# Performance work log

Hardware: AMD Instinct MI355X
Metric: run time of the kernel (lower is better)

The kernel has to match this reference:

```python
import jax, jax.numpy as jnp
import numpy as np
from jax import lax

B, C_IN, H, W = 4, 64, 128, 128
NUM_HIDDEN = 64
KSIZE = 3
DIST = 1
MOVES = 2 * DIST + 1          # 3
MOVESQ = MOVES * MOVES        # 9
TIME_STEPS = 8
LOSS_WEIGHT = 0.01


def _shift(a, dy, dx):
    """out(y, x) = a(y+dy, x+dx), zero outside; dy,dx in {-1,0,1}. a: [..., H, W]."""
    p = jnp.pad(a, [(0, 0)] * (a.ndim - 2) + [(1, 1), (1, 1)])
    h, w = a.shape[-2], a.shape[-1]
    return p[..., 1 + dy:1 + dy + h, 1 + dx:1 + dx + w]


def _gather(o4):
    # gather_kernel[i,0,i//3,i%3]=1 => channel i is o4 shifted by (i//3-1, i%3-1)
    return jnp.stack([_shift(o4, i // MOVES - 1, i % MOVES - 1) for i in range(MOVESQ)], axis=1)


def _merge(hxo):
    # hxo: [B, nh, 9, H, W]; merge_kernel[0, 9-i-1, i//3, i%3]=1 grouped per hidden channel
    # => merged(y,x) = sum_j hxo[:,:,j](y + 1 - j//3, x + 1 - j%3)
    return sum(_shift(hxo[:, :, j], 1 - j // MOVES, 1 - j % MOVES) for j in range(MOVESQ))


def _forward(x, mask, w_ih, b_ih, w_hh, b_hh, w_ho, b_ho):
    b, _, h, w = x.shape
    pad = KSIZE // 2
    i_all = lax.conv_general_dilated(
        x, w_ih, (1, 1), [(pad, pad), (pad, pad)],
        dimension_numbers=("NCHW", "OIHW", "NCHW")) + b_ih[None, :, None, None]
    i_r, i_i, i_n = jnp.split(i_all, 3, axis=1)

    h0 = jnp.zeros((b, NUM_HIDDEN, h, w), x.dtype)
    loss0 = jnp.zeros((b, MOVESQ, h, w), x.dtype)  # scalar init broadcasts to this shape

    def step(carry, _):
        hid, loss = carry
        hh = jnp.einsum("bchw,oc->bohw", hid, w_hh) + b_hh[None, :, None, None]
        h_r, h_i, h_n = jnp.split(hh, 3, axis=1)
        resetgate = jax.nn.sigmoid(i_r + h_r)
        inputgate = jax.nn.sigmoid(i_i + h_i)
        newgate = jnp.tanh(i_n + resetgate * h_n)
        hy = newgate + inputgate * (hid - newgate)
        o = jax.nn.softmax(jnp.einsum("bchw,oc->bohw", hy, w_ho) + b_ho[None, :, None, None], axis=1)
        o4 = o[:, 4]
        diff = (_gather(o4) - o) ** 2 * o
        bce = -jnp.mean(mask * jnp.log(1.0 - o4) + (1.0 - mask) * jnp.log(o4))
        loss = loss + bce + diff * LOSS_WEIGHT
        hxo = jnp.einsum("bchw,bdhw->bcdhw", hy, o)  # [B, nh, 9, H, W]
        h_next = _merge(hxo)
        return (h_next, loss), (h_next, o)

    (_, loss), (hiddens, outs) = lax.scan(step, (h0, loss0), None, length=TIME_STEPS)
    return hiddens, outs, loss


def setup_inputs() -> dict:
    key = jax.random.key(0)
    ks = jax.random.split(key, 8)
    s = 0.05
    return {
        "x": jax.random.normal(ks[0], (B, C_IN, H, W), jnp.float32),
        "mask": jax.random.uniform(ks[1], (B, H, W), jnp.float32),
        "w_ih": jax.random.normal(ks[2], (3 * NUM_HIDDEN, C_IN, KSIZE, KSIZE), jnp.float32) * s,
        "b_ih": jax.random.normal(ks[3], (3 * NUM_HIDDEN,), jnp.float32) * s,
        "w_hh": jax.random.normal(ks[4], (3 * NUM_HIDDEN, NUM_HIDDEN), jnp.float32) * s,
        "b_hh": jax.random.normal(ks[5], (3 * NUM_HIDDEN,), jnp.float32) * s,
        "w_ho": jax.random.normal(ks[6], (MOVESQ, NUM_HIDDEN), jnp.float32) * s,
        "b_ho": jax.random.normal(ks[7], (MOVESQ,), jnp.float32) * s,
    }


def reference(x, mask, w_ih, b_ih, w_hh, b_hh, w_ho, b_ho):
    return _forward(x, mask, w_ih, b_ih, w_hh, b_hh, w_ho, b_ho)
```

## Files before the change

### kernel.cpp

```cpp
#include <hip/hip_runtime.h>

#define NP 16384
#define HID_SZ 4194304
#define O_SZ   589824
#define OUTS_OFF 33554432
#define LOSS_OFF 38273024

#define WS_IALL0 0
#define WS_IALL1 4194304
#define WS_HYA   6291456
#define WS_HYB   8388624
#define WS_WHH   10485792
#define WS_WHOB  10491936
#define WS_BTF   10492448
#define WS_BCEP  10547744
#define WS_BCET  10555936

typedef __attribute__((ext_vector_type(8))) short bf16x8;
typedef __attribute__((ext_vector_type(8))) unsigned short ushort8;
typedef __attribute__((ext_vector_type(4))) unsigned short usht4;
typedef __attribute__((ext_vector_type(4))) float f32x4;

__device__ __forceinline__ float frcp(float x) { return __builtin_amdgcn_rcpf(x); }
__device__ __forceinline__ unsigned short f2bf(float f) {
    unsigned int u = __float_as_uint(f);
    return (unsigned short)((u + 0x7fffu + ((u >> 16) & 1u)) >> 16);
}
__device__ __forceinline__ float bf2f(unsigned short h) {
    return __uint_as_float(((unsigned int)h) << 16);
}
__device__ __forceinline__ int swz_bid(int bid) { return ((bid & 7) << 7) | (bid >> 3); }

__global__ __launch_bounds__(256) void prep_all(const float* __restrict__ x,
                                                const float* __restrict__ w_hh,
                                                const float* __restrict__ w_ho,
                                                const float* __restrict__ w_ih,
                                                unsigned short* __restrict__ xTh,
                                                unsigned short* __restrict__ whhBf,
                                                unsigned short* __restrict__ whoBf,
                                                unsigned short* __restrict__ BTf) {
    const int tid = threadIdx.x;
    if (blockIdx.x < 256) {
        const int p = blockIdx.x * 256 + tid;
        const int b = p >> 14, yx = p & 16383;
        const size_t base = ((size_t)p) << 6;
        for (int ic0 = 0; ic0 < 64; ic0 += 8) {
            ushort8 vh;
#pragma unroll
            for (int j = 0; j < 8; ++j)
                vh[j] = f2bf(x[(((size_t)(b * 64 + ic0 + j)) << 14) + yx]);
            *(ushort8*)(xTh + base + ic0) = vh;
        }
    } else {
        int i = (blockIdx.x - 256) * 256 + tid;
        if (i < 12288) {
            int f = i >> 9, r = i & 511;
            int lane = r >> 3, e = r & 7, lrow = lane & 15, lkq = lane >> 4;
            int ih = f / 12, n = f % 12;
            whhBf[i] = f2bf(w_hh[(n * 16 + lrow) * 64 + ih * 32 + lkq * 8 + e]);
        } else if (i < 13312) {
            int j = i - 12288;
            int f = j >> 9, r = j & 511;
            int lane = r >> 3, e = r & 7, lrow = lane & 15, lkq = lane >> 4;
            whoBf[j] = (lrow < 9) ? f2bf(w_ho[lrow * 64 + f * 32 + lkq * 8 + e]) : (unsigned short)0;
        } else if (i < 13312 + 110592) {
            int k2 = i - 13312;
            int f = k2 >> 9, r = k2 & 511;
            int lane = r >> 3, e = r & 7, lrow = lane & 15, lkq = lane >> 4;
            int tapih = f / 12, n = f % 12;
            int tap = tapih >> 1, ih = tapih & 1;
            int oc = n * 16 + lrow, ic = ih * 32 + lkq * 8 + e;
            BTf[k2] = f2bf(w_ih[(oc * 64 + ic) * 9 + tap]);
        }
    }
}

__global__ __launch_bounds__(256, 4) void conv_mfma(const unsigned short* __restrict__ xTh,
                                                    const unsigned short* __restrict__ BTf,
                                                    const float* __restrict__ b_ih,
                                                    unsigned short* __restrict__ iall0,
                                                    unsigned short* __restrict__ iall1) {
    __shared__ __align__(16) unsigned char smem[25344];
    const int tid = threadIdx.x;
    const int bid = swz_bid(blockIdx.x);
    const int b = bid >> 8, y = (bid >> 1) & 127, hh2 = bid & 1;

    for (int ch = tid; ch < 1584; ch += 256) {
        const int row = ch / 528;
        const int rem = ch - row * 528;
        const int pxl = rem >> 3, icc = rem & 7;
        const int gy = y + row - 1, gx = hh2 * 64 + pxl - 1;
        ushort8 vh = {};
        if (gy >= 0 && gy < 128 && gx >= 0 && gx < 128) {
            const size_t go = ((size_t)(b * 16384 + gy * 128 + gx)) * 64 + icc * 8;
            vh = *(const ushort8*)(xTh + go);
        }
        const int off = ((row * 66 + pxl) * 128 + icc * 16) ^ ((pxl & 7) << 4);
        *(ushort8*)(smem + off) = vh;
    }
    __syncthreads();

    const int lane = tid & 63, wv = tid >> 6;
    const int lrow = lane & 15, lkq = lane >> 4;
    const unsigned short* BTl = BTf + lane * 8;

    f32x4 acc[12] = {};
#pragma unroll
    for (int tap = 0; tap < 9; ++tap) {
        const int row = tap / 3, dx = tap % 3 - 1;
#pragma unroll
        for (int ih = 0; ih < 2; ++ih) {
            const int pxl = wv * 16 + lrow + dx + 1;
            const int off = ((row * 66 + pxl) * 128 + ih * 64 + lkq * 16) ^ ((pxl & 7) << 4);
            bf16x8 Ah = *(const bf16x8*)(smem + off);
#pragma unroll
            for (int n = 0; n < 12; ++n) {
                bf16x8 Bh = *(const bf16x8*)(BTl + (((tap * 2 + ih) * 12 + n) << 9));
                acc[n] = __builtin_amdgcn_mfma_f32_16x16x32_bf16(Ah, Bh, acc[n], 0, 0, 0);
            }
        }
    }

    float bias[12];
#pragma unroll
    for (int n = 0; n < 12; ++n) bias[n] = b_ih[n * 16 + lrow];
    const size_t rowb = (size_t)((b * 128 + y) * 2 + hh2);
#pragma unroll
    for (int r = 0; r < 4; ++r) {
        ushort8 v0;
        usht4 v1;
#pragma unroll
        for (int n = 0; n < 8; ++n) v0[n] = f2bf(acc[n][r] + bias[n]);
#pragma unroll
        for (int n = 8; n < 12; ++n) v1[n - 8] = f2bf(acc[n][r] + bias[n]);
        *(ushort8*)(iall0 + (rowb << 13) + ((wv * 4 + r) << 9) + lane * 8) = v0;
        *(usht4*)(iall1 + (rowb << 12) + ((wv * 4 + r) << 8) + lane * 4) = v1;
    }
}

template <bool FIRST>
__global__ __launch_bounds__(256, 4) void step_kernel(const unsigned short* __restrict__ hyp,
                                                      const float* __restrict__ o_prev,
                                                      const unsigned short* __restrict__ iall0,
                                                      const unsigned short* __restrict__ iall1,
                                                      const unsigned short* __restrict__ whhBf,
                                                      const float* __restrict__ b_hh,
                                                      const unsigned short* __restrict__ whoBf,
                                                      const float* __restrict__ b_ho,
                                                      const float* __restrict__ mask,
                                                      float* __restrict__ hidd_out,
                                                      unsigned short* __restrict__ hy_cur,
                                                      float* __restrict__ o_out,
                                                      float* __restrict__ bceP) {
    __shared__ __align__(16) unsigned char smem[19904];
    float* ostrip = (float*)(smem + 8192);
    unsigned short* hy_p = (unsigned short*)(smem + 10656);
    float* red = (float*)(smem + 19872);

    const int tid = threadIdx.x;
    const int bid = swz_bid(blockIdx.x);
    const int b = bid >> 8, y = (bid >> 1) & 127, hh2 = bid & 1;
    const int pxb = hh2 * 64, yxrow = y * 128;

    if constexpr (!FIRST) {
        const int c = tid >> 2, pq = tid & 3;
        const int gx0 = pxb + pq * 16;
        const unsigned short* hb = hyp + (((size_t)(b * 64 + c)) << 14);
        ushort8 w8[3][4];
#pragma unroll
        for (int r = 0; r < 3; ++r) {
            const int gyc = min(max(y + r - 1, 0), 127);
            const unsigned short* src = hb + gyc * 128 + gx0 - 8;
#pragma unroll
            for (int q = 0; q < 4; ++q) w8[r][q] = *(const ushort8*)(src + q * 8);
        }
        const float* ob = o_prev + (((size_t)b * 9) << 14);
        for (int e = tid; e < 594; e += 256) {
            const int j = e / 66, s = e - j * 66;
            const int rj = y + 1 - j / 3;
            const int gx = pxb - 1 + s;
            const bool ok = (rj >= 0) && (rj < 128) && (gx >= 0) && (gx < 128);
            ostrip[j * 68 + s] = ok ? ob[(((size_t)j) << 14) + rj * 128 + gx] : 0.0f;
        }
        __syncthreads();

        float a[16];
#pragma unroll
        for (int px = 0; px < 16; ++px) a[px] = 0.0f;
#pragma unroll
        for (int r = 0; r < 3; ++r) {
            float wf[18];
#pragma unroll
            for (int k = 0; k < 18; ++k)
                wf[k] = bf2f((unsigned short)w8[r][(k + 7) >> 3][(k + 7) & 7]);
#pragma unroll
            for (int ex = -1; ex <= 1; ++ex) {
                const int idx = r * 3 + (ex + 1);
                const int j = 8 - idx;
                const float* osj = ostrip + j * 68 + pq * 16 + 1 + ex;
#pragma unroll
                for (int px = 0; px < 16; ++px)
                    a[px] = fmaf(wf[px + ex + 1], osj[px], a[px]);
            }
        }
        const size_t hob = (((size_t)(b * 64 + c)) << 14) + yxrow + gx0;
#pragma unroll
        for (int q = 0; q < 4; ++q) {
            f32x4 v = {a[q * 4], a[q * 4 + 1], a[q * 4 + 2], a[q * 4 + 3]};
            *(f32x4*)(hidd_out + hob + q * 4) = v;
        }
#pragma unroll
        for (int px = 0; px < 16; ++px) {
            const int pxl = pq * 16 + px;
            *(unsigned short*)(smem + ((pxl * 128 + c * 2) ^ ((pxl & 7) << 4))) = f2bf(a[px]);
        }
        __syncthreads();
    }

    const int lane = tid & 63, wv = tid >> 6;
    const int lrow = lane & 15, lkq = lane >> 4;

    f32x4 acc[12] = {};
    if constexpr (!FIRST) {
        bf16x8 Ah[2];
#pragma unroll
        for (int ih = 0; ih < 2; ++ih) {
            const int pxa = wv * 16 + lrow;
            const int off = (pxa * 128 + ih * 64 + lkq * 16) ^ ((pxa & 7) << 4);
            Ah[ih] = *(const bf16x8*)(smem + off);
        }
#pragma unroll
        for (int ih = 0; ih < 2; ++ih)
#pragma unroll
            for (int n = 0; n < 12; ++n) {
                bf16x8 Bh = *(const bf16x8*)(whhBf + (((ih * 12 + n) << 9) + lane * 8));
                acc[n] = __builtin_amdgcn_mfma_f32_16x16x32_bf16(Ah[ih], Bh, acc[n], 0, 0, 0);
            }
    }

    float bhr[4], bhi[4], bhn[4];
#pragma unroll
    for (int nf = 0; nf < 4; ++nf) {
        bhr[nf] = b_hh[nf * 16 + lrow];
        bhi[nf] = b_hh[64 + nf * 16 + lrow];
        bhn[nf] = b_hh[128 + nf * 16 + lrow];
    }
    const size_t rowb = (size_t)((b * 128 + y) * 2 + hh2);
    const unsigned short* p0 = iall0 + (rowb << 13) + (wv << 11) + lane * 8;
    const unsigned short* p1 = iall1 + (rowb << 12) + (wv << 10) + lane * 4;
    ushort8 lo[4];
    usht4 hi[4];
#pragma unroll
    for (int rr = 0; rr < 4; ++rr) {
        lo[rr] = *(const ushort8*)(p0 + (rr << 9));
        hi[rr] = *(const usht4*)(p1 + (rr << 8));
    }
#pragma unroll
    for (int nf = 0; nf < 4; ++nf) {
        const int g = nf * 16 + lrow;
        usht4 hv4;
#pragma unroll
        for (int rr = 0; rr < 4; ++rr) {
            const int pxl = wv * 16 + lkq * 4 + rr;
            float hr = bhr[nf], hig = bhi[nf], hn = bhn[nf];
            if constexpr (!FIRST) {
                hr += acc[nf][rr];
                hig += acc[nf + 4][rr];
                hn += acc[nf + 8][rr];
            }
            float ir = bf2f(lo[rr][nf]), ii = bf2f(lo[rr][4 + nf]), inn = bf2f(hi[rr][nf]);
            float rg = frcp(1.0f + __expf(-(ir + hr)));
            float ig = frcp(1.0f + __expf(-(ii + hig)));
            float t2 = __expf(2.0f * (inn + rg * hn));
            float nn = 1.0f - 2.0f * frcp(t2 + 1.0f);
            float hp = 0.0f;
            if constexpr (!FIRST) {
                const int offA = (pxl * 128 + g * 2) ^ ((pxl & 7) << 4);
                hp = bf2f(*(const unsigned short*)(smem + offA));
            }
            unsigned short hv = f2bf(nn + ig * (hp - nn));
            hy_p[pxl * 72 + g] = hv;
            hv4[rr] = hv;
        }
        *(usht4*)(hy_cur + (((size_t)(b * 64 + g)) << 14) + yxrow + pxb + wv * 16 + lkq * 4) = hv4;
    }
    __syncthreads();

    f32x4 aco = {};
#pragma unroll
    for (int ih = 0; ih < 2; ++ih) {
        const int pxa = wv * 16 + lrow;
        bf16x8 Ao = *(const bf16x8*)(hy_p + pxa * 72 + ih * 32 + lkq * 8);
        bf16x8 Bo = *(const bf16x8*)(whoBf + ((ih << 9) + lane * 8));
        aco = __builtin_amdgcn_mfma_f32_16x16x32_bf16(Ao, Bo, aco, 0, 0, 0);
    }
    const float bho = (lrow < 9) ? b_ho[lrow] : 0.0f;
    float ov[4];
    float vbce = 0.0f;
    const int yx0 = yxrow + pxb + wv * 16 + lkq * 4;
#pragma unroll
    for (int r = 0; r < 4; ++r) {
        float lg = aco[r] + bho;
        float v = (lrow < 9) ? lg : -1e30f;
        v = fmaxf(v, __shfl_xor(v, 1));
        v = fmaxf(v, __shfl_xor(v, 2));
        v = fmaxf(v, __shfl_xor(v, 4));
        v = fmaxf(v, __shfl_xor(v, 8));
        float e = (lrow < 9) ? __expf(lg - v) : 0.0f;
        float s = e;
        s += __shfl_xor(s, 1);
        s += __shfl_xor(s, 2);
        s += __shfl_xor(s, 4);
        s += __shfl_xor(s, 8);
        ov[r] = e * frcp(s);
    }
    if (lrow < 9) {
        f32x4 wvec = {ov[0], ov[1], ov[2], ov[3]};
        *(f32x4*)(o_out + (((size_t)(b * 9 + lrow)) << 14) + yx0) = wvec;
    }
    if (lrow == 4) {
        const f32x4 mk = *(const f32x4*)(mask + (((size_t)b) << 14) + yx0);
#pragma unroll
        for (int r = 0; r < 4; ++r)
            vbce += mk[r] * __logf(1.0f - ov[r]) + (1.0f - mk[r]) * __logf(ov[r]);
    }
    float v = (lrow == 4) ? vbce : 0.0f;
#pragma unroll
    for (int d = 1; d < 64; d <<= 1) v += __shfl_xor(v, d);
    if (lane == 0) red[wv] = v;
    __syncthreads();
    if (tid == 0) bceP[bid] = red[0] + red[1] + red[2] + red[3];
}

__global__ __launch_bounds__(256) void final_fused(const unsigned short* __restrict__ hyp,
                                                   const float* __restrict__ o_all,
                                                   const float* __restrict__ bceP,
                                                   float* __restrict__ hidd7,
                                                   float* __restrict__ loss) {
    __shared__ __align__(16) float ostrip[9 * 68];
    __shared__ float o4s[3 * 68];
    __shared__ float redsh[256];
    const int tid = threadIdx.x;
    const int bid = swz_bid(blockIdx.x);
    const int b = bid >> 8, y = (bid >> 1) & 127, hh2 = bid & 1;
    const int pxb = hh2 * 64, yxrow = y * 128;

    float s = 0.0f;
    for (int i = tid; i < 8192; i += 256) s += bceP[i];
    redsh[tid] = s;
    __syncthreads();
    for (int off = 128; off > 0; off >>= 1) {
        if (tid < off) redsh[tid] += redsh[tid + off];
        __syncthreads();
    }
    const float bt = -redsh[0] * (1.0f / 65536.0f);

    {
        const int c = tid >> 2, pq = tid & 3;
        const int gx0 = pxb + pq * 16;
        const float* ob = o_all + (size_t)7 * O_SZ + (((size_t)b * 9) << 14);
        for (int e = tid; e < 594; e += 256) {
            const int j = e / 66, ss = e - j * 66;
            const int rj = y + 1 - j / 3;
            const int gx = pxb - 1 + ss;
            const bool ok = (rj >= 0) && (rj < 128) && (gx >= 0) && (gx < 128);
            ostrip[j * 68 + ss] = ok ? ob[(((size_t)j) << 14) + rj * 128 + gx] : 0.0f;
        }
        __syncthreads();
        const unsigned short* hb = hyp + (((size_t)(b * 64 + c)) << 14);
        float a[16];
#pragma unroll
        for (int px = 0; px < 16; ++px) a[px] = 0.0f;
#pragma unroll
        for (int r = 0; r < 3; ++r) {
            const int gyc = min(max(y + r - 1, 0), 127);
            const unsigned short* src = hb + gyc * 128 + gx0 - 8;
            ushort8 w8[4];
#pragma unroll
            for (int q = 0; q < 4; ++q) w8[q] = *(const ushort8*)(src + q * 8);
            float wf[18];
#pragma unroll
            for (int k = 0; k < 18; ++k)
                wf[k] = bf2f((unsigned short)w8[(k + 7) >> 3][(k + 7) & 7]);
#pragma unroll
            for (int ex = -1; ex <= 1; ++ex) {
                const int j = 8 - (r * 3 + (ex + 1));
                const float* osj = ostrip + j * 68 + pq * 16 + 1 + ex;
#pragma unroll
                for (int px = 0; px < 16; ++px)
                    a[px] = fmaf(wf[px + ex + 1], osj[px], a[px]);
            }
        }
        const size_t hob = (((size_t)(b * 64 + c)) << 14) + yxrow + gx0;
#pragma unroll
        for (int q = 0; q < 4; ++q) {
            f32x4 v = {a[q * 4], a[q * 4 + 1], a[q * 4 + 2], a[q * 4 + 3]};
            *(f32x4*)(hidd7 + hob + q * 4) = v;
        }
    }

    const int px = tid & 63, tq = tid >> 6;
    const int yx = yxrow + pxb + px;
    const int i0 = tq, i1 = tq + 4;
    float a0 = 0.0f, a1 = 0.0f, a2 = 0.0f;
    for (int t = 0; t < 8; ++t) {
        const float* ot = o_all + (size_t)t * O_SZ + (((size_t)b * 9) << 14);
        __syncthreads();
        for (int e = tid; e < 198; e += 256) {
            const int r = e / 66, ss = e - r * 66;
            const int ry = y + r - 1, gx = pxb - 1 + ss;
            const bool ok = (ry >= 0) && (ry < 128) && (gx >= 0) && (gx < 128);
            o4s[r * 68 + ss] = ok ? ot[(((size_t)4) << 14) + ry * 128 + gx] : 0.0f;
        }
        __syncthreads();
        {
            const float oi = ot[(((size_t)i0) << 14) + yx];
            const float g = o4s[(i0 / 3) * 68 + px + 1 + (i0 % 3 - 1)];
            const float d = g - oi;
            a0 = fmaf(d * d, oi, a0);
        }
        {
            const float oi = ot[(((size_t)i1) << 14) + yx];
            const float g = o4s[(i1 / 3) * 68 + px + 1 + (i1 % 3 - 1)];
            const float d = g - oi;
            a1 = fmaf(d * d, oi, a1);
        }
        if (tq == 0) {
            const float oi = ot[(((size_t)8) << 14) + yx];
            const float g = o4s[2 * 68 + px + 2];
            const float d = g - oi;
            a2 = fmaf(d * d, oi, a2);
        }
    }
    loss[(((size_t)(b * 9 + i0)) << 14) + yx] = a0 * 0.01f + bt;
    loss[(((size_t)(b * 9 + i1)) << 14) + yx] = a1 * 0.01f + bt;
    if (tq == 0) loss[(((size_t)(b * 9 + 8)) << 14) + yx] = a2 * 0.01f + bt;
}

extern "C" void kernel_launch(void* const* d_in, const int* in_sizes, int n_in,
                              void* d_out, int out_size, void* d_ws, size_t ws_size,
                              hipStream_t stream) {
    const float* x    = (const float*)d_in[0];
    const float* mask = (const float*)d_in[1];
    const float* w_ih = (const float*)d_in[2];
    const float* b_ih = (const float*)d_in[3];
    const float* w_hh = (const float*)d_in[4];
    const float* b_hh = (const float*)d_in[5];
    const float* w_ho = (const float*)d_in[6];
    const float* b_ho = (const float*)d_in[7];
    float* out = (float*)d_out;
    float* ws  = (float*)d_ws;

    unsigned short* iall0 = (unsigned short*)(ws + WS_IALL0);
    unsigned short* iall1 = (unsigned short*)(ws + WS_IALL1);
    unsigned short* xTh   = (unsigned short*)(ws + WS_HYA);
    unsigned short* hyA   = (unsigned short*)(ws + WS_HYA + 8);
    unsigned short* hyB   = (unsigned short*)(ws + WS_HYB + 8);
    unsigned short* whhBf = (unsigned short*)(ws + WS_WHH);
    unsigned short* whoBf = (unsigned short*)(ws + WS_WHOB);
    unsigned short* BTf   = (unsigned short*)(ws + WS_BTF);
    float* bceP = ws + WS_BCEP;
    float* lossp = out + LOSS_OFF;

    prep_all<<<740, 256, 0, stream>>>(x, w_hh, w_ho, w_ih, xTh, whhBf, whoBf, BTf);
    conv_mfma<<<1024, 256, 0, stream>>>(xTh, BTf, b_ih, iall0, iall1);

    step_kernel<true><<<1024, 256, 0, stream>>>(nullptr, nullptr, iall0, iall1, whhBf, b_hh,
                                                whoBf, b_ho, mask, nullptr, hyA,
                                                out + OUTS_OFF, bceP);
    for (int t = 1; t < 8; ++t) {
        const unsigned short* hypr = (t & 1) ? hyA : hyB;
        unsigned short* hyc = (t & 1) ? hyB : hyA;
        step_kernel<false><<<1024, 256, 0, stream>>>(hypr, out + OUTS_OFF + (size_t)(t - 1) * O_SZ,
                                                     iall0, iall1, whhBf, b_hh, whoBf, b_ho, mask,
                                                     out + (size_t)(t - 1) * HID_SZ, hyc,
                                                     out + OUTS_OFF + (size_t)t * O_SZ,
                                                     bceP + t * 1024);
    }
    final_fused<<<1024, 256, 0, stream>>>(hyB, out + OUTS_OFF, bceP,
                                          out + (size_t)7 * HID_SZ, lossp);
}
```

Before: 255.9 us.

## Fuse first GRU step into input convolution kernel

Merges the first recurrent step (gate math with zero hidden state, output projection, softmax, BCE partials) into the conv kernel. The gate inputs are used directly from registers, so step 0 no longer rereads them from global memory and one launch is removed. The workspace is re-laid out so the transposed input buffer no longer aliases a hidden-state buffer, which the fusion requires. The trade-off is higher register pressure and more shared-memory work in the conv kernel.

```diff
diff --git a/kernel.cpp b/kernel.cpp
--- a/kernel.cpp
+++ b/kernel.cpp
@@ -8,13 +8,13 @@
 
 #define WS_IALL0 0
 #define WS_IALL1 4194304
-#define WS_HYA   6291456
-#define WS_HYB   8388624
-#define WS_WHH   10485792
-#define WS_WHOB  10491936
-#define WS_BTF   10492448
-#define WS_BCEP  10547744
-#define WS_BCET  10555936
+#define WS_XTH   6291456
+#define WS_HYA   8388608
+#define WS_HYB   10485776
+#define WS_WHH   12582944
+#define WS_WHOB  12589088
+#define WS_BTF   12589600
+#define WS_BCEP  12644896
 
 typedef __attribute__((ext_vector_type(8))) short bf16x8;
 typedef __attribute__((ext_vector_type(8))) unsigned short ushort8;
@@ -75,21 +75,31 @@
     }
 }
 
-__global__ __launch_bounds__(256, 4) void conv_mfma(const unsigned short* __restrict__ xTh,
-                                                    const unsigned short* __restrict__ BTf,
-                                                    const float* __restrict__ b_ih,
-                                                    unsigned short* __restrict__ iall0,
-                                                    unsigned short* __restrict__ iall1) {
+__global__ __launch_bounds__(256, 4) void conv_step0(const unsigned short* __restrict__ xTh,
+                                                     const unsigned short* __restrict__ BTf,
+                                                     const float* __restrict__ b_ih,
+                                                     const float* __restrict__ b_hh,
+                                                     const unsigned short* __restrict__ whoBf,
+                                                     const float* __restrict__ b_ho,
+                                                     const float* __restrict__ mask,
+                                                     unsigned short* __restrict__ iall0,
+                                                     unsigned short* __restrict__ iall1,
+                                                     unsigned short* __restrict__ hy_cur,
+                                                     float* __restrict__ o_out,
+                                                     float* __restrict__ bceP) {
     __shared__ __align__(16) unsigned char smem[25344];
+    unsigned short* hy_p = (unsigned short*)(smem + 10656);
+    float* red = (float*)(smem + 19872);
     const int tid = threadIdx.x;
     const int bid = swz_bid(blockIdx.x);
     const int b = bid >> 8, y = (bid >> 1) & 127, hh2 = bid & 1;
+    const int pxb = hh2 * 64, yxrow = y * 128;
 
     for (int ch = tid; ch < 1584; ch += 256) {
         const int row = ch / 528;
         const int rem = ch - row * 528;
         const int pxl = rem >> 3, icc = rem & 7;
-        const int gy = y + row - 1, gx = hh2 * 64 + pxl - 1;
+        const int gy = y + row - 1, gx = pxb + pxl - 1;
         ushort8 vh = {};
         if (gy >= 0 && gy < 128 && gx >= 0 && gx < 128) {
             const size_t go = ((size_t)(b * 16384 + gy * 128 + gx)) * 64 + icc * 8;
@@ -125,20 +135,92 @@
 #pragma unroll
     for (int n = 0; n < 12; ++n) bias[n] = b_ih[n * 16 + lrow];
     const size_t rowb = (size_t)((b * 128 + y) * 2 + hh2);
+    ushort8 v0[4];
+    usht4 v1[4];
 #pragma unroll
     for (int r = 0; r < 4; ++r) {
-        ushort8 v0;
-        usht4 v1;
-#pragma unroll
-        for (int n = 0; n < 8; ++n) v0[n] = f2bf(acc[n][r] + bias[n]);
-#pragma unroll
-        for (int n = 8; n < 12; ++n) v1[n - 8] = f2bf(acc[n][r] + bias[n]);
-        *(ushort8*)(iall0 + (rowb << 13) + ((wv * 4 + r) << 9) + lane * 8) = v0;
-        *(usht4*)(iall1 + (rowb << 12) + ((wv * 4 + r) << 8) + lane * 4) = v1;
-    }
-}
-
-template <bool FIRST>
+#pragma unroll
+        for (int n = 0; n < 8; ++n) v0[r][n] = f2bf(acc[n][r] + bias[n]);
+#pragma unroll
+        for (int n = 8; n < 12; ++n) v1[r][n - 8] = f2bf(acc[n][r] + bias[n]);
+        *(ushort8*)(iall0 + (rowb << 13) + ((wv * 4 + r) << 9) + lane * 8) = v0[r];
+        *(usht4*)(iall1 + (rowb << 12) + ((wv * 4 + r) << 8) + lane * 4) = v1[r];
+    }
+    __syncthreads();
+
+    float bhr[4], bhi[4], bhn[4];
+#pragma unroll
+    for (int nf = 0; nf < 4; ++nf) {
+        bhr[nf] = b_hh[nf * 16 + lrow];
+        bhi[nf] = b_hh[64 + nf * 16 + lrow];
+        bhn[nf] = b_hh[128 + nf * 16 + lrow];
+    }
+#pragma unroll
+    for (int nf = 0; nf < 4; ++nf) {
+        const int g = nf * 16 + lrow;
+        usht4 hv4;
+#pragma unroll
+        for (int rr = 0; rr < 4; ++rr) {
+            const int pxl = wv * 16 + lkq * 4 + rr;
+            float ir = bf2f(v0[rr][nf]), ii = bf2f(v0[rr][4 + nf]), inn = bf2f(v1[rr][nf]);
+            float rg = frcp(1.0f + __expf(-(ir + bhr[nf])));
+            float ig = frcp(1.0f + __expf(-(ii + bhi[nf])));
+            float t2 = __expf(2.0f * (inn + rg * bhn[nf]));
+            float nn = 1.0f - 2.0f * frcp(t2 + 1.0f);
+            unsigned short hv = f2bf(nn + ig * (0.0f - nn));
+            hy_p[pxl * 72 + g] = hv;
+            hv4[rr] = hv;
+        }
+        *(usht4*)(hy_cur + (((size_t)(b * 64 + g)) << 14) + yxrow + pxb + wv * 16 + lkq * 4) = hv4;
+    }
+    __syncthreads();
+
+    f32x4 aco = {};
+#pragma unroll
+    for (int ih = 0; ih < 2; ++ih) {
+        const int pxa = wv * 16 + lrow;
+        bf16x8 Ao = *(const bf16x8*)(hy_p + pxa * 72 + ih * 32 + lkq * 8);
+        bf16x8 Bo = *(const bf16x8*)(whoBf + ((ih << 9) + lane * 8));
+        aco = __builtin_amdgcn_mfma_f32_16x16x32_bf16(Ao, Bo, aco, 0, 0, 0);
+    }
+    const float bho = (lrow < 9) ? b_ho[lrow] : 0.0f;
+    float ov[4];
+    float vbce = 0.0f;
+    const int yx0 = yxrow + pxb + wv * 16 + lkq * 4;
+#pragma unroll
+    for (int r = 0; r < 4; ++r) {
+        float lg = aco[r] + bho;
+        float v = (lrow < 9) ? lg : -1e30f;
+        v = fmaxf(v, __shfl_xor(v, 1));
+        v = fmaxf(v, __shfl_xor(v, 2));
+        v = fmaxf(v, __shfl_xor(v, 4));
+        v = fmaxf(v, __shfl_xor(v, 8));
+        float e = (lrow < 9) ? __expf(lg - v) : 0.0f;
+        float s = e;
+        s += __shfl_xor(s, 1);
+        s += __shfl_xor(s, 2);
+        s += __shfl_xor(s, 4);
+        s += __shfl_xor(s, 8);
+        ov[r] = e * frcp(s);
+    }
+    if (lrow < 9) {
+        f32x4 wvec = {ov[0], ov[1], ov[2], ov[3]};
+        *(f32x4*)(o_out + (((size_t)(b * 9 + lrow)) << 14) + yx0) = wvec;
+    }
+    if (lrow == 4) {
+        const f32x4 mk = *(const f32x4*)(mask + (((size_t)b) << 14) + yx0);
+#pragma unroll
+        for (int r = 0; r < 4; ++r)
+            vbce += mk[r] * __logf(1.0f - ov[r]) + (1.0f - mk[r]) * __logf(ov[r]);
+    }
+    float v = (lrow == 4) ? vbce : 0.0f;
+#pragma unroll
+    for (int d = 1; d < 64; d <<= 1) v += __shfl_xor(v, d);
+    if (lane == 0) red[wv] = v;
+    __syncthreads();
+    if (tid == 0) bceP[bid] = red[0] + red[1] + red[2] + red[3];
+}
+
 __global__ __launch_bounds__(256, 4) void step_kernel(const unsigned short* __restrict__ hyp,
                                                       const float* __restrict__ o_prev,
                                                       const unsigned short* __restrict__ iall0,
@@ -162,7 +244,7 @@
     const int b = bid >> 8, y = (bid >> 1) & 127, hh2 = bid & 1;
     const int pxb = hh2 * 64, yxrow = y * 128;
 
-    if constexpr (!FIRST) {
+    {
         const int c = tid >> 2, pq = tid & 3;
         const int gx0 = pxb + pq * 16;
         const unsigned short* hb = hyp + (((size_t)(b * 64 + c)) << 14);
@@ -221,7 +303,7 @@
     const int lrow = lane & 15, lkq = lane >> 4;
 
     f32x4 acc[12] = {};
-    if constexpr (!FIRST) {
+    {
         bf16x8 Ah[2];
 #pragma unroll
         for (int ih = 0; ih < 2; ++ih) {
@@ -262,22 +344,16 @@
 #pragma unroll
         for (int rr = 0; rr < 4; ++rr) {
             const int pxl = wv * 16 + lkq * 4 + rr;
-            float hr = bhr[nf], hig = bhi[nf], hn = bhn[nf];
-            if constexpr (!FIRST) {
-                hr += acc[nf][rr];
-                hig += acc[nf + 4][rr];
-                hn += acc[nf + 8][rr];
-            }
+            float hr = bhr[nf] + acc[nf][rr];
+            float hig = bhi[nf] + acc[nf + 4][rr];
+            float hn = bhn[nf] + acc[nf + 8][rr];
             float ir = bf2f(lo[rr][nf]), ii = bf2f(lo[rr][4 + nf]), inn = bf2f(hi[rr][nf]);
             float rg = frcp(1.0f + __expf(-(ir + hr)));
             float ig = frcp(1.0f + __expf(-(ii + hig)));
             float t2 = __expf(2.0f * (inn + rg * hn));
             float nn = 1.0f - 2.0f * frcp(t2 + 1.0f);
-            float hp = 0.0f;
-            if constexpr (!FIRST) {
-                const int offA = (pxl * 128 + g * 2) ^ ((pxl & 7) << 4);
-                hp = bf2f(*(const unsigned short*)(smem + offA));
-            }
+            const int offA = (pxl * 128 + g * 2) ^ ((pxl & 7) << 4);
+            float hp = bf2f(*(const unsigned short*)(smem + offA));
             unsigned short hv = f2bf(nn + ig * (hp - nn));
             hy_p[pxl * 72 + g] = hv;
             hv4[rr] = hv;
@@ -453,9 +529,9 @@
 
     unsigned short* iall0 = (unsigned short*)(ws + WS_IALL0);
     unsigned short* iall1 = (unsigned short*)(ws + WS_IALL1);
-    unsigned short* xTh   = (unsigned short*)(ws + WS_HYA);
-    unsigned short* hyA   = (unsigned short*)(ws + WS_HYA + 8);
-    unsigned short* hyB   = (unsigned short*)(ws + WS_HYB + 8);
+    unsigned short* xTh   = (unsigned short*)(ws + WS_XTH);
+    unsigned short* hyA   = (unsigned short*)(ws + WS_HYA) + 8;
+    unsigned short* hyB   = (unsigned short*)(ws + WS_HYB) + 8;
     unsigned short* whhBf = (unsigned short*)(ws + WS_WHH);
     unsigned short* whoBf = (unsigned short*)(ws + WS_WHOB);
     unsigned short* BTf   = (unsigned short*)(ws + WS_BTF);
@@ -463,19 +539,16 @@
     float* lossp = out + LOSS_OFF;
 
     prep_all<<<740, 256, 0, stream>>>(x, w_hh, w_ho, w_ih, xTh, whhBf, whoBf, BTf);
-    conv_mfma<<<1024, 256, 0, stream>>>(xTh, BTf, b_ih, iall0, iall1);
-
-    step_kernel<true><<<1024, 256, 0, stream>>>(nullptr, nullptr, iall0, iall1, whhBf, b_hh,
-                                                whoBf, b_ho, mask, nullptr, hyA,
-                                                out + OUTS_OFF, bceP);
+    conv_step0<<<1024, 256, 0, stream>>>(xTh, BTf, b_ih, b_hh, whoBf, b_ho, mask,
+                                         iall0, iall1, hyA, out + OUTS_OFF, bceP);
     for (int t = 1; t < 8; ++t) {
         const unsigned short* hypr = (t & 1) ? hyA : hyB;
         unsigned short* hyc = (t & 1) ? hyB : hyA;
-        step_kernel<false><<<1024, 256, 0, stream>>>(hypr, out + OUTS_OFF + (size_t)(t - 1) * O_SZ,
-                                                     iall0, iall1, whhBf, b_hh, whoBf, b_ho, mask,
-                                                     out + (size_t)(t - 1) * HID_SZ, hyc,
-                                                     out + OUTS_OFF + (size_t)t * O_SZ,
-                                                     bceP + t * 1024);
+        step_kernel<<<1024, 256, 0, stream>>>(hypr, out + OUTS_OFF + (size_t)(t - 1) * O_SZ,
+                                              iall0, iall1, whhBf, b_hh, whoBf, b_ho, mask,
+                                              out + (size_t)(t - 1) * HID_SZ, hyc,
+                                              out + OUTS_OFF + (size_t)t * O_SZ,
+                                              bceP + t * 1024);
     }
     final_fused<<<1024, 256, 0, stream>>>(hyB, out + OUTS_OFF, bceP,
                                           out + (size_t)7 * HID_SZ, lossp);
```

Result: faster. 225.6 us (-11.8%).
